# Performance work log

Measured on AMD Instinct MI355X. Metric: run time of the kernel, lower is better.

## Reference

```python
import jax, jax.numpy as jnp
import numpy as np

B, T, C, H = 8, 2048, 768, 64  # batch, block_size, n_embd, head_size

def setup_inputs() -> dict:
    key = jax.random.key(0)
    kx, kk, kq, kv = jax.random.split(key, 4)
    x = jax.random.normal(kx, (B, T, C), dtype=jnp.float32)
    Wk = jax.random.normal(kk, (C, H), dtype=jnp.float32) * (C ** -0.5)
    Wq = jax.random.normal(kq, (C, H), dtype=jnp.float32) * (C ** -0.5)
    Wv = jax.random.normal(kv, (C, H), dtype=jnp.float32) * (C ** -0.5)
    return {"x": x, "Wk": Wk, "Wq": Wq, "Wv": Wv}

def reference(x, Wk, Wq, Wv):
    # single causal self-attention head (dropout in eval mode = identity)
    k = jnp.einsum('btc,ch->bth', x, Wk)  # [B,T,H]
    q = jnp.einsum('btc,ch->bth', x, Wq)
    v = jnp.einsum('btc,ch->bth', x, Wv)
    scale = jnp.asarray(k.shape[-1], x.dtype) ** -0.5
    wei = jnp.einsum('bth,bsh->bts', q, k) * scale  # [B,T,T]
    t = x.shape[1]
    causal = jnp.tril(jnp.ones((t, t), dtype=bool))
    wei = jnp.where(causal[None, :, :], wei, jnp.asarray(-jnp.inf, wei.dtype))
    wei = jax.nn.softmax(wei, axis=-1)
    out = jnp.einsum('bts,bsh->bth', wei, v)  # [B,T,H]
    return out
```

## Files before the change

### kernel.cpp

```cpp
#include <hip/hip_runtime.h>
#include <hip/hip_bf16.h>

typedef __attribute__((ext_vector_type(8))) short short8;
typedef __attribute__((ext_vector_type(4))) float f32x4;

#define B_  8
#define T_  2048
#define C_  768
#define H_  64
#define M_  (B_ * T_)

#define GLDS16(g, l) __builtin_amdgcn_global_load_lds(                        \
    (const __attribute__((address_space(1))) void*)(g),                       \
    (__attribute__((address_space(3))) void*)(l), 16, 0, 0)

static __device__ __forceinline__ unsigned short f2bf(float f) {
    __hip_bfloat16 h = __float2bfloat16(f);
    return *reinterpret_cast<unsigned short*>(&h);
}

static __device__ __forceinline__ short8 make_frag(const unsigned short* p0, const unsigned short* p1) {
    const ushort4 a = *reinterpret_cast<const ushort4*>(p0);
    const ushort4 b = *reinterpret_cast<const ushort4*>(p1);
    short8 r;
    r[0] = (short)a.x; r[1] = (short)a.y; r[2] = (short)a.z; r[3] = (short)a.w;
    r[4] = (short)b.x; r[5] = (short)b.y; r[6] = (short)b.z; r[7] = (short)b.w;
    return r;
}

static __device__ __forceinline__ int swz(int row, int u) {
    return row * 64 + ((((u) >> 3) ^ (row & 7)) << 3) + (u & 7);
}

static __device__ __forceinline__ int fragoff(int k) {
    const int half = k >> 5;
    const int kk   = k & 31;
    const int c    = half * 4 + ((kk >> 2) & 3);
    const int p    = (kk & 3) + ((kk & 16) >> 2);
    return c * 8 + p;
}

#define LOG2E_SCALE 0.18033688011112042f

__global__ __launch_bounds__(256) void prep_w(
    const float* __restrict__ Wq, const float* __restrict__ Wk, const float* __restrict__ Wv,
    unsigned short* __restrict__ Wt) {

    const int t   = threadIdx.x;
    const int mat = blockIdx.x / 48;
    const int kb  = blockIdx.x % 48;
    const int h   = t & 63;
    const int k0  = (kb * 4 + (t >> 6)) * 4;

    const float* Ws = (mat == 0) ? Wq : (mat == 1) ? Wk : Wv;
    const float sc  = (mat == 0) ? LOG2E_SCALE : 1.f;
    ushort4 o;
    o.x = f2bf(Ws[(size_t)(k0 + 0) * H_ + h] * sc);
    o.y = f2bf(Ws[(size_t)(k0 + 1) * H_ + h] * sc);
    o.z = f2bf(Ws[(size_t)(k0 + 2) * H_ + h] * sc);
    o.w = f2bf(Ws[(size_t)(k0 + 3) * H_ + h] * sc);
    *reinterpret_cast<ushort4*>(&Wt[(size_t)(mat * 64 + h) * C_ + k0]) = o;
}

__global__ __launch_bounds__(256) void proj_kernel(
    const float* __restrict__ x, const unsigned short* __restrict__ Wt,
    unsigned short* __restrict__ qkv) {

    __shared__ unsigned short Als[2][8192];

    const int tid = threadIdx.x;
    const int w   = tid >> 6;
    const int l   = tid & 63;
    const int lg  = l >> 4;
    const int lc  = l & 15;
    const int row0 = blockIdx.x * 64;

    const int sr   = tid >> 2;
    const int so   = tid & 3;
    const int srt  = sr >> 4;
    const int sr15 = sr & 15;
    const int sbase = (so * 16 + (sr15 ^ so)) * 8;

    f32x4 acc[4][3];
#pragma unroll
    for (int rt = 0; rt < 4; ++rt)
#pragma unroll
        for (int ct = 0; ct < 3; ++ct) acc[rt][ct] = (f32x4)0.f;

    const unsigned short* bbase[3];
#pragma unroll
    for (int ct = 0; ct < 3; ++ct)
        bbase[ct] = Wt + (size_t)(w * 48 + ct * 16 + lc) * C_ + lg * 8;

    const float* xrow = x + (size_t)(row0 + sr) * C_ + so * 8;

    float4 fa[4][2];
#pragma unroll
    for (int jj = 0; jj < 4; ++jj) {
        fa[jj][0] = *reinterpret_cast<const float4*>(xrow + jj * 32);
        fa[jj][1] = *reinterpret_cast<const float4*>(xrow + jj * 32 + 4);
    }

#pragma unroll
    for (int c = 0; c < 6; ++c) {
#pragma unroll
        for (int jj = 0; jj < 4; ++jj) {
            short8 v;
            v[0] = (short)f2bf(fa[jj][0].x); v[1] = (short)f2bf(fa[jj][0].y);
            v[2] = (short)f2bf(fa[jj][0].z); v[3] = (short)f2bf(fa[jj][0].w);
            v[4] = (short)f2bf(fa[jj][1].x); v[5] = (short)f2bf(fa[jj][1].y);
            v[6] = (short)f2bf(fa[jj][1].z); v[7] = (short)f2bf(fa[jj][1].w);
            *reinterpret_cast<short8*>(&Als[c & 1][(srt * 4 + jj) * 512 + sbase]) = v;
        }
        if (c < 5) {
#pragma unroll
            for (int jj = 0; jj < 4; ++jj) {
                fa[jj][0] = *reinterpret_cast<const float4*>(xrow + (c + 1) * 128 + jj * 32);
                fa[jj][1] = *reinterpret_cast<const float4*>(xrow + (c + 1) * 128 + jj * 32 + 4);
            }
        }
        __syncthreads();
#pragma unroll
        for (int kk = 0; kk < 4; ++kk) {
            short8 bcur[3];
#pragma unroll
            for (int ct = 0; ct < 3; ++ct)
                bcur[ct] = *reinterpret_cast<const short8*>(bbase[ct] + c * 128 + kk * 32);
            short8 af[4];
#pragma unroll
            for (int rt = 0; rt < 4; ++rt)
                af[rt] = *reinterpret_cast<const short8*>(
                    &Als[c & 1][(rt * 4 + kk) * 512 + (lg * 16 + (lc ^ lg)) * 8]);
#pragma unroll
            for (int rt = 0; rt < 4; ++rt)
#pragma unroll
                for (int ct = 0; ct < 3; ++ct)
                    acc[rt][ct] = __builtin_amdgcn_mfma_f32_16x16x32_bf16(af[rt], bcur[ct], acc[rt][ct], 0, 0, 0);
        }
    }

    __syncthreads();
    unsigned short* Ls = &Als[0][0];
#pragma unroll
    for (int ct = 0; ct < 3; ++ct) {
        const int col = w * 48 + ct * 16 + lc;
        const int mat = col >> 6;
        const int h   = col & 63;
        const int foh = fragoff(h);
#pragma unroll
        for (int rt = 0; rt < 4; ++rt)
#pragma unroll
            for (int j = 0; j < 4; ++j) {
                const int s6 = rt * 16 + lg * 4 + j;
                const unsigned short v = f2bf(acc[rt][ct][j]);
                if (mat == 0)      Ls[s6 * 64 + h] = v;
                else if (mat == 1) Ls[4096 + swz(s6, foh)] = v;
                else               Ls[8192 + swz(h, fragoff(s6))] = v;
            }
    }
    __syncthreads();

    unsigned short* Qd   = qkv;
    unsigned short* Kimg = qkv + (size_t)M_ * H_;
    unsigned short* Vimg = qkv + (size_t)2 * M_ * H_;
    const size_t g12 = (size_t)blockIdx.x << 12;
    const int o = tid * 8;
#pragma unroll
    for (int s = 0; s < 2; ++s) {
        const int off = s * 2048 + o;
        *reinterpret_cast<short8*>(&Qd[(size_t)row0 * 64 + off]) =
            *reinterpret_cast<const short8*>(&Ls[off]);
        *reinterpret_cast<short8*>(&Kimg[g12 + off]) =
            *reinterpret_cast<const short8*>(&Ls[4096 + off]);
        *reinterpret_cast<short8*>(&Vimg[g12 + off]) =
            *reinterpret_cast<const short8*>(&Ls[8192 + off]);
    }
}

#define SEG_FLOATS 4224

template<int SEG>
static __device__ __forceinline__ int segs_per_batch() { return SEG == 32 ? 32 : 80; }

template<int SEG>
static __device__ __forceinline__ void decode_seg(int r, int& qt, int& seg) {
    if (SEG == 32) { qt = r; seg = 0; return; }
    if (r < 8)       { qt = r;                seg = 0; }
    else if (r < 24) { qt = 8  + (r - 8) / 2; seg = (r - 8) & 1; }
    else if (r < 48) { qt = 16 + (r - 24) / 3; seg = (r - 24) % 3; }
    else             { qt = 24 + (r - 48) / 4; seg = (r - 48) & 3; }
}

template<int SEG>
static __device__ __forceinline__ int seg_prefix(int qt) {
    if (SEG == 32) return qt;
    if (qt < 8)  return qt;
    if (qt < 16) return 8  + 2 * (qt - 8);
    if (qt < 24) return 24 + 3 * (qt - 16);
    return 48 + 4 * (qt - 24);
}

template<int SEG>
__global__ __launch_bounds__(256) void attn_partial(
    const unsigned short* __restrict__ qkv, float* __restrict__ part,
    float* __restrict__ out) {

    const int spb = segs_per_batch<SEG>();
    const int b   = blockIdx.x / spb;
    const int rr  = spb - 1 - (blockIdx.x % spb);
    int qt, seg;
    decode_seg<SEG>(rr, qt, seg);

    const int tid = threadIdx.x;
    const int w  = tid >> 6;
    const int l  = tid & 63;
    const int lg = l >> 4;
    const int lc = l & 15;

    __shared__ unsigned short Kls[3][4096];
    __shared__ unsigned short Vls[3][4096];

    const unsigned short* Qg = qkv;
    const unsigned short* Kg = qkv + (size_t)M_ * H_;
    const unsigned short* Vg = qkv + (size_t)2 * M_ * H_;

    const unsigned short* qrow = Qg + (size_t)(b * T_ + qt * 64 + w * 16 + lc) * H_;
    short8 qf[2];
#pragma unroll
    for (int ks = 0; ks < 2; ++ks)
        qf[ks] = make_frag(qrow + ks * 32 + lg * 4, qrow + ks * 32 + lg * 4 + 16);

    float mval = -1e30f, lsum = 0.f;
    f32x4 oT[4];
#pragma unroll
    for (int t = 0; t < 4; ++t) oT[t] = (f32x4)0.f;

    const int q_glob = qt * 64 + w * 16 + lc;

    const int kv_beg = seg * SEG;
    const int kv_end = min(kv_beg + SEG, qt + 1);
    const int n      = kv_end - kv_beg;

    const int go = w * 1024 + l * 8;

    auto stage = [&](int buf, int kv) {
        const size_t tb = ((size_t)(b * 32 + kv)) << 12;
        const unsigned short* kt = Kg + tb;
        const unsigned short* vt = Vg + tb;
        GLDS16(kt + go,       &Kls[buf][w * 1024]);
        GLDS16(kt + go + 512, &Kls[buf][w * 1024 + 512]);
        GLDS16(vt + go,       &Vls[buf][w * 1024]);
        GLDS16(vt + go + 512, &Vls[buf][w * 1024 + 512]);
    };

    stage(0, kv_beg);
    if (n > 1) stage(1, kv_beg + 1);

    int b0 = 0;
    for (int i = 0; i < n; ++i) {
        __builtin_amdgcn_s_barrier();
        asm volatile("" ::: "memory");
        if (i + 2 < n) {
            stage((b0 + 2) % 3, kv_beg + i + 2);
            asm volatile("s_waitcnt vmcnt(8)" ::: "memory");
        } else if (i + 1 < n) {
            asm volatile("s_waitcnt vmcnt(4)" ::: "memory");
        } else {
            asm volatile("s_waitcnt vmcnt(0)" ::: "memory");
        }
        __builtin_amdgcn_s_barrier();
        asm volatile("" ::: "memory");

        const int kv = kv_beg + i;
        const unsigned short* Kc = Kls[b0];
        const unsigned short* Vc = Vls[b0];

        f32x4 sT[4];
#pragma unroll
        for (int st = 0; st < 4; ++st) {
            f32x4 accs = (f32x4)0.f;
#pragma unroll
            for (int ks = 0; ks < 2; ++ks) {
                const short8 kf = *reinterpret_cast<const short8*>(
                    &Kc[swz(st * 16 + lc, (ks * 4 + lg) * 8)]);
                accs = __builtin_amdgcn_mfma_f32_16x16x32_bf16(kf, qf[ks], accs, 0, 0, 0);
            }
            sT[st] = accs;
        }

        float p[4][4];
#pragma unroll
        for (int st = 0; st < 4; ++st)
#pragma unroll
            for (int r = 0; r < 4; ++r)
                p[st][r] = sT[st][r];

        if (kv == qt) {
#pragma unroll
            for (int st = 0; st < 4; ++st)
#pragma unroll
                for (int r = 0; r < 4; ++r)
                    if ((kv * 64 + st * 16 + lg * 4 + r) > q_glob) p[st][r] = -1e30f;
        }

        float pm[4];
#pragma unroll
        for (int st = 0; st < 4; ++st)
            pm[st] = fmaxf(fmaxf(p[st][0], p[st][1]), fmaxf(p[st][2], p[st][3]));
        float pmax = fmaxf(fmaxf(pm[0], pm[1]), fmaxf(pm[2], pm[3]));
        pmax = fmaxf(pmax, __shfl_xor(pmax, 16));
        pmax = fmaxf(pmax, __shfl_xor(pmax, 32));

        if (!__all(pmax <= mval)) {
            const float mnew  = fmaxf(mval, pmax);
            const float alpha = exp2f(mval - mnew);
            mval = mnew;
            lsum *= alpha;
#pragma unroll
            for (int ht = 0; ht < 4; ++ht) oT[ht] *= alpha;
        }

        float ps[4];
#pragma unroll
        for (int st = 0; st < 4; ++st) {
#pragma unroll
            for (int r = 0; r < 4; ++r)
                p[st][r] = exp2f(p[st][r] - mval);
            ps[st] = (p[st][0] + p[st][1]) + (p[st][2] + p[st][3]);
        }
        float srow = (ps[0] + ps[1]) + (ps[2] + ps[3]);
        srow += __shfl_xor(srow, 16);
        srow += __shfl_xor(srow, 32);
        lsum += srow;

        short8 pb[2];
#pragma unroll
        for (int ks = 0; ks < 2; ++ks) {
#pragma unroll
            for (int r = 0; r < 4; ++r) {
                pb[ks][r]     = (short)f2bf(p[2 * ks][r]);
                pb[ks][r + 4] = (short)f2bf(p[2 * ks + 1][r]);
            }
        }

#pragma unroll
        for (int ks = 0; ks < 2; ++ks) {
#pragma unroll
            for (int ht = 0; ht < 4; ++ht) {
                const short8 vf = *reinterpret_cast<const short8*>(
                    &Vc[swz(ht * 16 + lc, (ks * 4 + lg) * 8)]);
                oT[ht] = __builtin_amdgcn_mfma_f32_16x16x32_bf16(vf, pb[ks], oT[ht], 0, 0, 0);
            }
        }
        b0 = (b0 == 2) ? 0 : b0 + 1;
    }

    const int nseg = (SEG == 32) ? 1 : (qt / 8 + 1);
    if (nseg == 1) {
        const float inv = 1.f / lsum;
        float* op = out + (size_t)(b * T_ + q_glob) * H_;
#pragma unroll
        for (int ht = 0; ht < 4; ++ht) {
            f32x4 v = oT[ht] * inv;
            *reinterpret_cast<f32x4*>(&op[ht * 16 + lg * 4]) = v;
        }
    } else {
        float* base = part + (size_t)(b * spb + seg_prefix<SEG>(qt) + seg) * SEG_FLOATS;
#pragma unroll
        for (int ht = 0; ht < 4; ++ht)
            *reinterpret_cast<f32x4*>(&base[(w * 16 + lc) * 64 + ht * 16 + lg * 4]) = oT[ht];
        if (lg == 0) {
            base[4096 + w * 16 + lc] = mval;
            base[4160 + w * 16 + lc] = lsum;
        }
    }
}

__global__ __launch_bounds__(256) void attn_merge8(
    const float* __restrict__ part, float* __restrict__ out) {

    const int b  = blockIdx.x / 24;
    const int qt = 8 + blockIdx.x % 24;
    const int nseg = qt / 8 + 1;
    const float* base0 = part + (size_t)(b * 80 + seg_prefix<8>(qt)) * SEG_FLOATS;

    const int tid = threadIdx.x;
    const int row = tid >> 2;
    const int c0  = (tid & 3) * 16;

    float M = -1e30f;
    for (int s = 0; s < nseg; ++s)
        M = fmaxf(M, base0[(size_t)s * SEG_FLOATS + 4096 + row]);

    float L = 0.f;
    f32x4 acc[4];
#pragma unroll
    for (int k = 0; k < 4; ++k) acc[k] = (f32x4)0.f;

    for (int s = 0; s < nseg; ++s) {
        const float* sb = base0 + (size_t)s * SEG_FLOATS;
        const float wsc = exp2f(sb[4096 + row] - M);
        L += sb[4160 + row] * wsc;
#pragma unroll
        for (int k = 0; k < 4; ++k) {
            const f32x4 ov = *reinterpret_cast<const f32x4*>(&sb[row * 64 + c0 + 4 * k]);
            acc[k] += ov * wsc;
        }
    }
    const float inv = 1.f / L;
    float* op = out + (size_t)(b * T_ + qt * 64 + row) * H_ + c0;
#pragma unroll
    for (int k = 0; k < 4; ++k)
        *reinterpret_cast<f32x4*>(&op[4 * k]) = acc[k] * inv;
}

extern "C" void kernel_launch(void* const* d_in, const int* in_sizes, int n_in,
                              void* d_out, int out_size, void* d_ws, size_t ws_size,
                              hipStream_t stream) {
    const float* x  = (const float*)d_in[0];
    const float* Wk = (const float*)d_in[1];
    const float* Wq = (const float*)d_in[2];
    const float* Wv = (const float*)d_in[3];

    const size_t qkvB = (size_t)3 * M_ * H_ * 2;
    const size_t WtB  = (size_t)3 * H_ * C_ * 2;
    unsigned short* qkv = (unsigned short*)d_ws;
    unsigned short* Wt  = (unsigned short*)((char*)d_ws + qkvB);
    float* part = (float*)((char*)d_ws + qkvB + WtB);
    float* out  = (float*)d_out;

    prep_w<<<dim3(144), dim3(256), 0, stream>>>(Wq, Wk, Wv, Wt);
    proj_kernel<<<dim3(M_ / 64), dim3(256), 0, stream>>>(x, Wt, qkv);

    const size_t need8 = qkvB + WtB + (size_t)(B_ * 80) * SEG_FLOATS * 4;
    if (ws_size >= need8) {
        attn_partial<8><<<dim3(B_ * 80), dim3(256), 0, stream>>>(qkv, part, out);
        attn_merge8<<<dim3(B_ * 24), dim3(256), 0, stream>>>(part, out);
    } else {
        attn_partial<32><<<dim3(B_ * 32), dim3(256), 0, stream>>>(qkv, part, out);
    }
}
```

Baseline: 57.03 us.

## Pair adjacent query tiles per 512-thread block to share K/V staging

Replaces the per-query-tile split-KV attention kernel with one where each 512-thread block handles two adjacent 64-row query tiles, so every staged K/V tile in LDS serves both tiles. This roughly halves global-to-LDS traffic per query row and halves the number of blocks. The pipeline also moves from triple to double buffering, with all 8 waves sharing the staging work. The merge kernel is rewritten for the new partial layout. The risks are less overlap of loads with compute, fewer blocks to fill the device, and the even tile in each pair doing one wasted fully-masked KV tile on the diagonal.

```diff
diff --git a/kernel.cpp b/kernel.cpp
--- a/kernel.cpp
+++ b/kernel.cpp
@@ -178,38 +178,240 @@
 }
 
 #define SEG_FLOATS 4224
-
-template<int SEG>
-static __device__ __forceinline__ int segs_per_batch() { return SEG == 32 ? 32 : 80; }
-
-template<int SEG>
-static __device__ __forceinline__ void decode_seg(int r, int& qt, int& seg) {
-    if (SEG == 32) { qt = r; seg = 0; return; }
-    if (r < 8)       { qt = r;                seg = 0; }
-    else if (r < 24) { qt = 8  + (r - 8) / 2; seg = (r - 8) & 1; }
-    else if (r < 48) { qt = 16 + (r - 24) / 3; seg = (r - 24) % 3; }
-    else             { qt = 24 + (r - 48) / 4; seg = (r - 48) & 3; }
-}
-
-template<int SEG>
-static __device__ __forceinline__ int seg_prefix(int qt) {
-    if (SEG == 32) return qt;
-    if (qt < 8)  return qt;
-    if (qt < 16) return 8  + 2 * (qt - 8);
-    if (qt < 24) return 24 + 3 * (qt - 16);
-    return 48 + 4 * (qt - 24);
-}
-
-template<int SEG>
-__global__ __launch_bounds__(256) void attn_partial(
+#define SPB_PAIR 40
+
+static __device__ __forceinline__ void decode_pair(int r, int& pj, int& seg) {
+    if (r < 4)       { pj = r;                 seg = 0; }
+    else if (r < 12) { pj = 4  + (r - 4) / 2;  seg = (r - 4) & 1; }
+    else if (r < 24) { pj = 8  + (r - 12) / 3; seg = (r - 12) % 3; }
+    else             { pj = 12 + (r - 24) / 4; seg = (r - 24) & 3; }
+}
+
+static __device__ __forceinline__ int prefix_pair(int j) {
+    if (j < 4)  return j;
+    if (j < 8)  return 4  + 2 * (j - 4);
+    if (j < 12) return 12 + 3 * (j - 8);
+    return 24 + 4 * (j - 12);
+}
+
+__global__ __launch_bounds__(512) void attn_pair(
     const unsigned short* __restrict__ qkv, float* __restrict__ part,
     float* __restrict__ out) {
 
-    const int spb = segs_per_batch<SEG>();
-    const int b   = blockIdx.x / spb;
-    const int rr  = spb - 1 - (blockIdx.x % spb);
-    int qt, seg;
-    decode_seg<SEG>(rr, qt, seg);
+    const int b  = blockIdx.x / SPB_PAIR;
+    const int rr = SPB_PAIR - 1 - (blockIdx.x % SPB_PAIR);
+    int pj, seg;
+    decode_pair(rr, pj, seg);
+
+    const int tid  = threadIdx.x;
+    const int w    = tid >> 6;
+    const int w4   = w & 3;
+    const int half = w >> 2;
+    const int l    = tid & 63;
+    const int lg   = l >> 4;
+    const int lc   = l & 15;
+
+    const int qt  = pj * 2 + half;
+    const int qt1 = pj * 2 + 1;
+
+    __shared__ unsigned short Kls[2][4096];
+    __shared__ unsigned short Vls[2][4096];
+
+    const unsigned short* Qg = qkv;
+    const unsigned short* Kg = qkv + (size_t)M_ * H_;
+    const unsigned short* Vg = qkv + (size_t)2 * M_ * H_;
+
+    const unsigned short* qrow = Qg + (size_t)(b * T_ + qt * 64 + w4 * 16 + lc) * H_;
+    short8 qf[2];
+#pragma unroll
+    for (int ks = 0; ks < 2; ++ks)
+        qf[ks] = make_frag(qrow + ks * 32 + lg * 4, qrow + ks * 32 + lg * 4 + 16);
+
+    float mval = -1e30f, lsum = 0.f;
+    f32x4 oT[4];
+#pragma unroll
+    for (int t = 0; t < 4; ++t) oT[t] = (f32x4)0.f;
+
+    const int q_glob = qt * 64 + w4 * 16 + lc;
+
+    const int kv_beg = seg * 8;
+    const int kv_end = min(kv_beg + 8, qt1 + 1);
+    const int n      = kv_end - kv_beg;
+
+    const int go = w * 512 + l * 8;
+
+    auto stage = [&](int buf, int kv) {
+        const size_t tb = ((size_t)(b * 32 + kv)) << 12;
+        GLDS16(Kg + tb + go, &Kls[buf][w * 512]);
+        GLDS16(Vg + tb + go, &Vls[buf][w * 512]);
+    };
+
+    stage(0, kv_beg);
+    int cur = 0;
+
+    for (int i = 0; i < n; ++i) {
+        const int kv = kv_beg + i;
+        __builtin_amdgcn_s_barrier();
+        asm volatile("" ::: "memory");
+        if (i + 1 < n) {
+            stage(cur ^ 1, kv + 1);
+            asm volatile("s_waitcnt vmcnt(2)" ::: "memory");
+        } else {
+            asm volatile("s_waitcnt vmcnt(0)" ::: "memory");
+        }
+        __builtin_amdgcn_s_barrier();
+        asm volatile("" ::: "memory");
+
+        const unsigned short* Kc = Kls[cur];
+        const unsigned short* Vc = Vls[cur];
+
+        f32x4 sT[4];
+#pragma unroll
+        for (int st = 0; st < 4; ++st) {
+            f32x4 accs = (f32x4)0.f;
+#pragma unroll
+            for (int ks = 0; ks < 2; ++ks) {
+                const short8 kf = *reinterpret_cast<const short8*>(
+                    &Kc[swz(st * 16 + lc, (ks * 4 + lg) * 8)]);
+                accs = __builtin_amdgcn_mfma_f32_16x16x32_bf16(kf, qf[ks], accs, 0, 0, 0);
+            }
+            sT[st] = accs;
+        }
+
+        float p[4][4];
+#pragma unroll
+        for (int st = 0; st < 4; ++st)
+#pragma unroll
+            for (int r = 0; r < 4; ++r)
+                p[st][r] = sT[st][r];
+
+        if (kv >= qt) {
+#pragma unroll
+            for (int st = 0; st < 4; ++st)
+#pragma unroll
+                for (int r = 0; r < 4; ++r)
+                    if ((kv * 64 + st * 16 + lg * 4 + r) > q_glob) p[st][r] = -1e30f;
+        }
+
+        float pm[4];
+#pragma unroll
+        for (int st = 0; st < 4; ++st)
+            pm[st] = fmaxf(fmaxf(p[st][0], p[st][1]), fmaxf(p[st][2], p[st][3]));
+        float pmax = fmaxf(fmaxf(pm[0], pm[1]), fmaxf(pm[2], pm[3]));
+        pmax = fmaxf(pmax, __shfl_xor(pmax, 16));
+        pmax = fmaxf(pmax, __shfl_xor(pmax, 32));
+
+        if (!__all(pmax <= mval)) {
+            const float mnew  = fmaxf(mval, pmax);
+            const float alpha = exp2f(mval - mnew);
+            mval = mnew;
+            lsum *= alpha;
+#pragma unroll
+            for (int ht = 0; ht < 4; ++ht) oT[ht] *= alpha;
+        }
+
+        float ps[4];
+#pragma unroll
+        for (int st = 0; st < 4; ++st) {
+#pragma unroll
+            for (int r = 0; r < 4; ++r)
+                p[st][r] = exp2f(p[st][r] - mval);
+            ps[st] = (p[st][0] + p[st][1]) + (p[st][2] + p[st][3]);
+        }
+        float srow = (ps[0] + ps[1]) + (ps[2] + ps[3]);
+        srow += __shfl_xor(srow, 16);
+        srow += __shfl_xor(srow, 32);
+        lsum += srow;
+
+        short8 pb[2];
+#pragma unroll
+        for (int ks = 0; ks < 2; ++ks) {
+#pragma unroll
+            for (int r = 0; r < 4; ++r) {
+                pb[ks][r]     = (short)f2bf(p[2 * ks][r]);
+                pb[ks][r + 4] = (short)f2bf(p[2 * ks + 1][r]);
+            }
+        }
+
+#pragma unroll
+        for (int ks = 0; ks < 2; ++ks) {
+#pragma unroll
+            for (int ht = 0; ht < 4; ++ht) {
+                const short8 vf = *reinterpret_cast<const short8*>(
+                    &Vc[swz(ht * 16 + lc, (ks * 4 + lg) * 8)]);
+                oT[ht] = __builtin_amdgcn_mfma_f32_16x16x32_bf16(vf, pb[ks], oT[ht], 0, 0, 0);
+            }
+        }
+        cur ^= 1;
+    }
+
+    const int nseg = pj / 4 + 1;
+    if (nseg == 1) {
+        const float inv = 1.f / lsum;
+        float* op = out + (size_t)(b * T_ + q_glob) * H_;
+#pragma unroll
+        for (int ht = 0; ht < 4; ++ht) {
+            f32x4 v = oT[ht] * inv;
+            *reinterpret_cast<f32x4*>(&op[ht * 16 + lg * 4]) = v;
+        }
+    } else {
+        float* base = part +
+            (size_t)((b * SPB_PAIR + prefix_pair(pj) + seg) * 2 + half) * SEG_FLOATS;
+#pragma unroll
+        for (int ht = 0; ht < 4; ++ht)
+            *reinterpret_cast<f32x4*>(&base[(w4 * 16 + lc) * 64 + ht * 16 + lg * 4]) = oT[ht];
+        if (lg == 0) {
+            base[4096 + w4 * 16 + lc] = mval;
+            base[4160 + w4 * 16 + lc] = lsum;
+        }
+    }
+}
+
+__global__ __launch_bounds__(256) void attn_merge_p(
+    const float* __restrict__ part, float* __restrict__ out) {
+
+    const int b  = blockIdx.x / 24;
+    const int qt = 8 + blockIdx.x % 24;
+    const int pj = qt >> 1;
+    const int nseg = pj / 4 + 1;
+
+    const int tid = threadIdx.x;
+    const int row = tid >> 2;
+    const int c0  = (tid & 3) * 16;
+
+    const size_t slot0 = (size_t)((b * SPB_PAIR + prefix_pair(pj)) * 2 + (qt & 1));
+
+    float M = -1e30f;
+    for (int s = 0; s < nseg; ++s)
+        M = fmaxf(M, part[(slot0 + 2 * s) * SEG_FLOATS + 4096 + row]);
+
+    float L = 0.f;
+    f32x4 acc[4];
+#pragma unroll
+    for (int k = 0; k < 4; ++k) acc[k] = (f32x4)0.f;
+
+    for (int s = 0; s < nseg; ++s) {
+        const float* sb = part + (slot0 + 2 * s) * SEG_FLOATS;
+        const float wsc = exp2f(sb[4096 + row] - M);
+        L += sb[4160 + row] * wsc;
+#pragma unroll
+        for (int k = 0; k < 4; ++k) {
+            const f32x4 ov = *reinterpret_cast<const f32x4*>(&sb[row * 64 + c0 + 4 * k]);
+            acc[k] += ov * wsc;
+        }
+    }
+    const float inv = 1.f / L;
+    float* op = out + (size_t)(b * T_ + qt * 64 + row) * H_ + c0;
+#pragma unroll
+    for (int k = 0; k < 4; ++k)
+        *reinterpret_cast<f32x4*>(&op[4 * k]) = acc[k] * inv;
+}
+
+__global__ __launch_bounds__(256) void attn_single32(
+    const unsigned short* __restrict__ qkv, float* __restrict__ out) {
+
+    const int b  = blockIdx.x >> 5;
+    const int qt = 31 - (blockIdx.x & 31);
 
     const int tid = threadIdx.x;
     const int w  = tid >> 6;
@@ -217,8 +419,8 @@
     const int lg = l >> 4;
     const int lc = l & 15;
 
-    __shared__ unsigned short Kls[3][4096];
-    __shared__ unsigned short Vls[3][4096];
+    __shared__ unsigned short Kls[2][4096];
+    __shared__ unsigned short Vls[2][4096];
 
     const unsigned short* Qg = qkv;
     const unsigned short* Kg = qkv + (size_t)M_ * H_;
@@ -236,34 +438,24 @@
     for (int t = 0; t < 4; ++t) oT[t] = (f32x4)0.f;
 
     const int q_glob = qt * 64 + w * 16 + lc;
-
-    const int kv_beg = seg * SEG;
-    const int kv_end = min(kv_beg + SEG, qt + 1);
-    const int n      = kv_end - kv_beg;
-
     const int go = w * 1024 + l * 8;
 
     auto stage = [&](int buf, int kv) {
         const size_t tb = ((size_t)(b * 32 + kv)) << 12;
-        const unsigned short* kt = Kg + tb;
-        const unsigned short* vt = Vg + tb;
-        GLDS16(kt + go,       &Kls[buf][w * 1024]);
-        GLDS16(kt + go + 512, &Kls[buf][w * 1024 + 512]);
-        GLDS16(vt + go,       &Vls[buf][w * 1024]);
-        GLDS16(vt + go + 512, &Vls[buf][w * 1024 + 512]);
+        GLDS16(Kg + tb + go,       &Kls[buf][w * 1024]);
+        GLDS16(Kg + tb + go + 512, &Kls[buf][w * 1024 + 512]);
+        GLDS16(Vg + tb + go,       &Vls[buf][w * 1024]);
+        GLDS16(Vg + tb + go + 512, &Vls[buf][w * 1024 + 512]);
     };
 
-    stage(0, kv_beg);
-    if (n > 1) stage(1, kv_beg + 1);
-
-    int b0 = 0;
-    for (int i = 0; i < n; ++i) {
+    stage(0, 0);
+    int cur = 0;
+
+    for (int kv = 0; kv <= qt; ++kv) {
         __builtin_amdgcn_s_barrier();
         asm volatile("" ::: "memory");
-        if (i + 2 < n) {
-            stage((b0 + 2) % 3, kv_beg + i + 2);
-            asm volatile("s_waitcnt vmcnt(8)" ::: "memory");
-        } else if (i + 1 < n) {
+        if (kv < qt) {
+            stage(cur ^ 1, kv + 1);
             asm volatile("s_waitcnt vmcnt(4)" ::: "memory");
         } else {
             asm volatile("s_waitcnt vmcnt(0)" ::: "memory");
@@ -271,9 +463,8 @@
         __builtin_amdgcn_s_barrier();
         asm volatile("" ::: "memory");
 
-        const int kv = kv_beg + i;
-        const unsigned short* Kc = Kls[b0];
-        const unsigned short* Vc = Vls[b0];
+        const unsigned short* Kc = Kls[cur];
+        const unsigned short* Vc = Vls[cur];
 
         f32x4 sT[4];
 #pragma unroll
@@ -352,66 +543,16 @@
                 oT[ht] = __builtin_amdgcn_mfma_f32_16x16x32_bf16(vf, pb[ks], oT[ht], 0, 0, 0);
             }
         }
-        b0 = (b0 == 2) ? 0 : b0 + 1;
-    }
-
-    const int nseg = (SEG == 32) ? 1 : (qt / 8 + 1);
-    if (nseg == 1) {
-        const float inv = 1.f / lsum;
-        float* op = out + (size_t)(b * T_ + q_glob) * H_;
-#pragma unroll
-        for (int ht = 0; ht < 4; ++ht) {
-            f32x4 v = oT[ht] * inv;
-            *reinterpret_cast<f32x4*>(&op[ht * 16 + lg * 4]) = v;
-        }
-    } else {
-        float* base = part + (size_t)(b * spb + seg_prefix<SEG>(qt) + seg) * SEG_FLOATS;
-#pragma unroll
-        for (int ht = 0; ht < 4; ++ht)
-            *reinterpret_cast<f32x4*>(&base[(w * 16 + lc) * 64 + ht * 16 + lg * 4]) = oT[ht];
-        if (lg == 0) {
-            base[4096 + w * 16 + lc] = mval;
-            base[4160 + w * 16 + lc] = lsum;
-        }
-    }
-}
-
-__global__ __launch_bounds__(256) void attn_merge8(
-    const float* __restrict__ part, float* __restrict__ out) {
-
-    const int b  = blockIdx.x / 24;
-    const int qt = 8 + blockIdx.x % 24;
-    const int nseg = qt / 8 + 1;
-    const float* base0 = part + (size_t)(b * 80 + seg_prefix<8>(qt)) * SEG_FLOATS;
-
-    const int tid = threadIdx.x;
-    const int row = tid >> 2;
-    const int c0  = (tid & 3) * 16;
-
-    float M = -1e30f;
-    for (int s = 0; s < nseg; ++s)
-        M = fmaxf(M, base0[(size_t)s * SEG_FLOATS + 4096 + row]);
-
-    float L = 0.f;
-    f32x4 acc[4];
-#pragma unroll
-    for (int k = 0; k < 4; ++k) acc[k] = (f32x4)0.f;
-
-    for (int s = 0; s < nseg; ++s) {
-        const float* sb = base0 + (size_t)s * SEG_FLOATS;
-        const float wsc = exp2f(sb[4096 + row] - M);
-        L += sb[4160 + row] * wsc;
-#pragma unroll
-        for (int k = 0; k < 4; ++k) {
-            const f32x4 ov = *reinterpret_cast<const f32x4*>(&sb[row * 64 + c0 + 4 * k]);
-            acc[k] += ov * wsc;
-        }
-    }
-    const float inv = 1.f / L;
-    float* op = out + (size_t)(b * T_ + qt * 64 + row) * H_ + c0;
-#pragma unroll
-    for (int k = 0; k < 4; ++k)
-        *reinterpret_cast<f32x4*>(&op[4 * k]) = acc[k] * inv;
+        cur ^= 1;
+    }
+
+    const float inv = 1.f / lsum;
+    float* op = out + (size_t)(b * T_ + q_glob) * H_;
+#pragma unroll
+    for (int ht = 0; ht < 4; ++ht) {
+        f32x4 v = oT[ht] * inv;
+        *reinterpret_cast<f32x4*>(&op[ht * 16 + lg * 4]) = v;
+    }
 }
 
 extern "C" void kernel_launch(void* const* d_in, const int* in_sizes, int n_in,
@@ -432,11 +573,11 @@
     prep_w<<<dim3(144), dim3(256), 0, stream>>>(Wq, Wk, Wv, Wt);
     proj_kernel<<<dim3(M_ / 64), dim3(256), 0, stream>>>(x, Wt, qkv);
 
-    const size_t need8 = qkvB + WtB + (size_t)(B_ * 80) * SEG_FLOATS * 4;
-    if (ws_size >= need8) {
-        attn_partial<8><<<dim3(B_ * 80), dim3(256), 0, stream>>>(qkv, part, out);
-        attn_merge8<<<dim3(B_ * 24), dim3(256), 0, stream>>>(part, out);
+    const size_t needP = qkvB + WtB + (size_t)(B_ * SPB_PAIR * 2) * SEG_FLOATS * 4;
+    if (ws_size >= needP) {
+        attn_pair<<<dim3(B_ * SPB_PAIR), dim3(512), 0, stream>>>(qkv, part, out);
+        attn_merge_p<<<dim3(B_ * 24), dim3(256), 0, stream>>>(part, out);
     } else {
-        attn_partial<32><<<dim3(B_ * 32), dim3(256), 0, stream>>>(qkv, part, out);
-    }
-}
+        attn_single32<<<dim3(B_ * 32), dim3(256), 0, stream>>>(qkv, out);
+    }
+}
```

Result: slower. 59.24 us (+3.9%).

## Load K/V fragments directly from global memory instead of LDS triple-buffering

Applied to the files above, without the earlier changes.

Replaces the LDS triple-buffered K/V staging (global_load_lds with barriers and waitcnt) with per-lane direct global loads of K and V fragments into registers, using precomputed swizzled offsets that match the layout written by the projection kernel. This drops the LDS footprint and the two block-wide barriers per KV tile, and issues the V loads before the softmax to hide their latency. In exchange, each of the 4 waves fetches the same K/V tile separately from global/L2, which multiplies cache traffic, and there is no explicit prefetch of the next tile.

```diff
diff --git a/kernel.cpp b/kernel.cpp
--- a/kernel.cpp
+++ b/kernel.cpp
@@ -9,10 +9,6 @@
 #define C_  768
 #define H_  64
 #define M_  (B_ * T_)
-
-#define GLDS16(g, l) __builtin_amdgcn_global_load_lds(                        \
-    (const __attribute__((address_space(1))) void*)(g),                       \
-    (__attribute__((address_space(3))) void*)(l), 16, 0, 0)
 
 static __device__ __forceinline__ unsigned short f2bf(float f) {
     __hip_bfloat16 h = __float2bfloat16(f);
@@ -201,7 +197,7 @@
 }
 
 template<int SEG>
-__global__ __launch_bounds__(256) void attn_partial(
+__global__ __launch_bounds__(256) void attn_direct(
     const unsigned short* __restrict__ qkv, float* __restrict__ part,
     float* __restrict__ out) {
 
@@ -217,9 +213,6 @@
     const int lg = l >> 4;
     const int lc = l & 15;
 
-    __shared__ unsigned short Kls[3][4096];
-    __shared__ unsigned short Vls[3][4096];
-
     const unsigned short* Qg = qkv;
     const unsigned short* Kg = qkv + (size_t)M_ * H_;
     const unsigned short* Vg = qkv + (size_t)2 * M_ * H_;
@@ -230,6 +223,13 @@
     for (int ks = 0; ks < 2; ++ks)
         qf[ks] = make_frag(qrow + ks * 32 + lg * 4, qrow + ks * 32 + lg * 4 + 16);
 
+    int fo[2][4];
+#pragma unroll
+    for (int x = 0; x < 2; ++x)
+#pragma unroll
+        for (int y = 0; y < 4; ++y)
+            fo[x][y] = swz(y * 16 + lc, (x * 4 + lg) * 8);
+
     float mval = -1e30f, lsum = 0.f;
     f32x4 oT[4];
 #pragma unroll
@@ -239,54 +239,34 @@
 
     const int kv_beg = seg * SEG;
     const int kv_end = min(kv_beg + SEG, qt + 1);
-    const int n      = kv_end - kv_beg;
-
-    const int go = w * 1024 + l * 8;
-
-    auto stage = [&](int buf, int kv) {
+
+    for (int kv = kv_beg; kv < kv_end; ++kv) {
         const size_t tb = ((size_t)(b * 32 + kv)) << 12;
-        const unsigned short* kt = Kg + tb;
-        const unsigned short* vt = Vg + tb;
-        GLDS16(kt + go,       &Kls[buf][w * 1024]);
-        GLDS16(kt + go + 512, &Kls[buf][w * 1024 + 512]);
-        GLDS16(vt + go,       &Vls[buf][w * 1024]);
-        GLDS16(vt + go + 512, &Vls[buf][w * 1024 + 512]);
-    };
-
-    stage(0, kv_beg);
-    if (n > 1) stage(1, kv_beg + 1);
-
-    int b0 = 0;
-    for (int i = 0; i < n; ++i) {
-        __builtin_amdgcn_s_barrier();
-        asm volatile("" ::: "memory");
-        if (i + 2 < n) {
-            stage((b0 + 2) % 3, kv_beg + i + 2);
-            asm volatile("s_waitcnt vmcnt(8)" ::: "memory");
-        } else if (i + 1 < n) {
-            asm volatile("s_waitcnt vmcnt(4)" ::: "memory");
-        } else {
-            asm volatile("s_waitcnt vmcnt(0)" ::: "memory");
-        }
-        __builtin_amdgcn_s_barrier();
-        asm volatile("" ::: "memory");
-
-        const int kv = kv_beg + i;
-        const unsigned short* Kc = Kls[b0];
-        const unsigned short* Vc = Vls[b0];
+        const unsigned short* Kt = Kg + tb;
+        const unsigned short* Vt = Vg + tb;
+
+        short8 kf[2][4];
+#pragma unroll
+        for (int ks = 0; ks < 2; ++ks)
+#pragma unroll
+            for (int st = 0; st < 4; ++st)
+                kf[ks][st] = *reinterpret_cast<const short8*>(&Kt[fo[ks][st]]);
 
         f32x4 sT[4];
 #pragma unroll
         for (int st = 0; st < 4; ++st) {
             f32x4 accs = (f32x4)0.f;
-#pragma unroll
-            for (int ks = 0; ks < 2; ++ks) {
-                const short8 kf = *reinterpret_cast<const short8*>(
-                    &Kc[swz(st * 16 + lc, (ks * 4 + lg) * 8)]);
-                accs = __builtin_amdgcn_mfma_f32_16x16x32_bf16(kf, qf[ks], accs, 0, 0, 0);
-            }
+            accs = __builtin_amdgcn_mfma_f32_16x16x32_bf16(kf[0][st], qf[0], accs, 0, 0, 0);
+            accs = __builtin_amdgcn_mfma_f32_16x16x32_bf16(kf[1][st], qf[1], accs, 0, 0, 0);
             sT[st] = accs;
         }
+
+        short8 vf[2][4];
+#pragma unroll
+        for (int ks = 0; ks < 2; ++ks)
+#pragma unroll
+            for (int ht = 0; ht < 4; ++ht)
+                vf[ks][ht] = *reinterpret_cast<const short8*>(&Vt[fo[ks][ht]]);
 
         float p[4][4];
 #pragma unroll
@@ -344,15 +324,10 @@
         }
 
 #pragma unroll
-        for (int ks = 0; ks < 2; ++ks) {
-#pragma unroll
-            for (int ht = 0; ht < 4; ++ht) {
-                const short8 vf = *reinterpret_cast<const short8*>(
-                    &Vc[swz(ht * 16 + lc, (ks * 4 + lg) * 8)]);
-                oT[ht] = __builtin_amdgcn_mfma_f32_16x16x32_bf16(vf, pb[ks], oT[ht], 0, 0, 0);
-            }
-        }
-        b0 = (b0 == 2) ? 0 : b0 + 1;
+        for (int ks = 0; ks < 2; ++ks)
+#pragma unroll
+            for (int ht = 0; ht < 4; ++ht)
+                oT[ht] = __builtin_amdgcn_mfma_f32_16x16x32_bf16(vf[ks][ht], pb[ks], oT[ht], 0, 0, 0);
     }
 
     const int nseg = (SEG == 32) ? 1 : (qt / 8 + 1);
@@ -434,9 +409,9 @@
 
     const size_t need8 = qkvB + WtB + (size_t)(B_ * 80) * SEG_FLOATS * 4;
     if (ws_size >= need8) {
-        attn_partial<8><<<dim3(B_ * 80), dim3(256), 0, stream>>>(qkv, part, out);
+        attn_direct<8><<<dim3(B_ * 80), dim3(256), 0, stream>>>(qkv, part, out);
         attn_merge8<<<dim3(B_ * 24), dim3(256), 0, stream>>>(part, out);
     } else {
-        attn_partial<32><<<dim3(B_ * 32), dim3(256), 0, stream>>>(qkv, part, out);
-    }
-}
+        attn_direct<32><<<dim3(B_ * 32), dim3(256), 0, stream>>>(qkv, part, out);
+    }
+}
```

Result: no change. 58.14 us (+1.9%).
